# Kernel tuning notes

Measured on AMD Instinct MI355X. Metric: run time of the kernel, lower is better.

The kernel has to match this reference:

```python
import jax, jax.numpy as jnp
import numpy as np
import math

# Model hyperparameters (SchNet defaults)
H = 128        # hidden_channels
F = 128        # num_filters
G = 50         # num_gaussians
CUT = 6.0      # cutoff (Angstrom)
L_INT = 3      # num_interactions
# Graph scale
N_MOL = 512    # molecules
APM = 32       # atoms per molecule
N = N_MOL * APM
BOX = 10.0     # side of cubic box per molecule


def _ssp(x):
    # ShiftedSoftplus
    return jax.nn.softplus(x) - math.log(2.0)


def setup_inputs() -> dict:
    rng = np.random.default_rng(0)
    pos = rng.uniform(0.0, BOX, (N_MOL, APM, 3)).astype(np.float32)
    # radius graph within each molecule (faithful to radius_graph_custom,
    # precomputed here because edge count is data-dependent)
    srcs, dsts = [], []
    for m in range(N_MOL):
        p = pos[m]
        dm = np.linalg.norm(p[:, None, :] - p[None, :, :], axis=-1)
        mask = dm <= CUT
        np.fill_diagonal(mask, False)
        s, t = np.nonzero(mask)
        srcs.append(s + m * APM)
        dsts.append(t + m * APM)
    edge_index = np.stack([np.concatenate(srcs), np.concatenate(dsts)]).astype(np.int32)
    pos = pos.reshape(N, 3)
    batch = np.repeat(np.arange(N_MOL, dtype=np.int32), APM)
    z = rng.integers(1, 100, N).astype(np.int32)

    key = jax.random.key(0)
    ks = jax.random.split(key, 16)
    s = 0.1
    nrm = lambda k, shp: (jax.random.normal(k, shp, dtype=jnp.float32) * s)
    return {
        "z": jnp.asarray(z),
        "pos": jnp.asarray(pos),
        "batch": jnp.asarray(batch),
        "edge_index": jnp.asarray(edge_index),
        "emb": nrm(ks[0], (100, H)),
        "mlp_w1": nrm(ks[1], (L_INT, G, F)),
        "mlp_b1": jnp.zeros((L_INT, F), jnp.float32),
        "mlp_w2": nrm(ks[2], (L_INT, F, F)),
        "mlp_b2": jnp.zeros((L_INT, F), jnp.float32),
        "cf1_w": nrm(ks[3], (L_INT, H, F)),
        "cf2_w": nrm(ks[4], (L_INT, F, H)),
        "cf2_b": jnp.zeros((L_INT, H), jnp.float32),
        "lin_w": nrm(ks[5], (L_INT, H, H)),
        "lin_b": jnp.zeros((L_INT, H), jnp.float32),
        "out1_w": nrm(ks[6], (H, H // 2)),
        "out1_b": jnp.zeros((H // 2,), jnp.float32),
        "out2_w": nrm(ks[7], (H // 2, 1)),
        "out2_b": jnp.zeros((1,), jnp.float32),
    }


def reference(z, pos, batch, edge_index, emb,
              mlp_w1, mlp_b1, mlp_w2, mlp_b2,
              cf1_w, cf2_w, cf2_b, lin_w, lin_b,
              out1_w, out1_b, out2_w, out2_b):
    src, dst = edge_index[0], edge_index[1]
    # edge_weight = euclidean distance (== cdist[src, dst])
    d = jnp.sqrt(jnp.sum((pos[src] - pos[dst]) ** 2, axis=-1))  # [E]
    # GaussianSmearing
    offs = jnp.linspace(0.0, CUT, G)
    coeff = -0.5 / (CUT / (G - 1)) ** 2
    edge_attr = jnp.exp(coeff * (d[:, None] - offs[None, :]) ** 2)  # [E, G]
    # cosine cutoff
    Ccut = 0.5 * (jnp.cos(d * math.pi / CUT) + 1.0)  # [E]

    h = emb[z]  # [N, H]
    for l in range(L_INT):
        # edge filter MLP with cutoff
        W = _ssp(edge_attr @ mlp_w1[l] + mlp_b1[l]) @ mlp_w2[l] + mlp_b2[l]  # [E, F]
        W = W * Ccut[:, None]
        # CFConv: lin1 -> gather x_j -> multiply -> scatter-add to dst -> lin2
        msg = (h @ cf1_w[l])[src] * W                                # [E, F]
        agg = jax.ops.segment_sum(msg, dst, num_segments=N)          # [N, F]
        v = agg @ cf2_w[l] + cf2_b[l]                                # [N, H]
        v = _ssp(v)
        v = v @ lin_w[l] + lin_b[l]
        h = h + v  # residual

    h = _ssp(h @ out1_w + out1_b)
    h = h @ out2_w + out2_b                                          # [N, 1]
    out = jax.ops.segment_sum(h, batch, num_segments=N_MOL)          # [N_MOL, 1]
    return out
```

## Files before the change

kernel.cpp:

```cpp
#include <hip/hip_runtime.h>
#include <hip/hip_bf16.h>
#include <math.h>

#define NATOMS 16384
#define NMOL   512
#define APM    32
#define GDIM   50
#define KTAB   2048
#define MAXEPM 1000

#define STRH 132
#define STRA 136

typedef __attribute__((ext_vector_type(8))) short   short8;
typedef __attribute__((ext_vector_type(4))) float   floatx4;

__device__ __forceinline__ float ssp(float x) {
    float e = __expf(-fabsf(x));
    return fmaxf(x, 0.0f) + __logf(1.0f + e) - 0.69314718055994531f;
}

__device__ __forceinline__ unsigned short f2bf(float x) {
    union { float f; unsigned int u; } v; v.f = x;
    unsigned int lsb = (v.u >> 16) & 1u;
    v.u += 0x7fffu + lsb;
    return (unsigned short)(v.u >> 16);
}

__device__ __forceinline__ float bf2f(unsigned int u16bits) {
    union { unsigned int u; float f; } v; v.u = u16bits << 16;
    return v.f;
}

__device__ __forceinline__ unsigned int pk2bf(float a, float b) {
    __hip_bfloat162 h = __float22bfloat162_rn(make_float2(a, b));
    unsigned int u;
    __builtin_memcpy(&u, &h, 4);
    return u;
}

#define KW1 72
#define KW2 136
#define TILE_K 63
#define NTILE 33

__global__ __launch_bounds__(256) void mega_setup_kernel(
    const float* __restrict__ pos, const int* __restrict__ eidx, int E, int EB,
    int* __restrict__ rowptr,
    const float* __restrict__ cf1, const float* __restrict__ cf2,
    const float* __restrict__ lin, const float* __restrict__ out1,
    unsigned short* __restrict__ Wtall, uint2* __restrict__ meta,
    const float* __restrict__ w1_, const float* __restrict__ b1_,
    const float* __restrict__ w2_, const float* __restrict__ b2_,
    unsigned int* __restrict__ Tp)
{
    const int WB = (9 * 16384 + 64 * 128 + 255) / 256;
    const int b = blockIdx.x;
    const int tid = threadIdx.x;

    if (b < EB) {
        int idx = b * 256 + tid;
        if (idx < E) {
            int s = eidx[idx], t = eidx[E + idx];
            float dx = pos[3 * s]     - pos[3 * t];
            float dy = pos[3 * s + 1] - pos[3 * t + 1];
            float dz = pos[3 * s + 2] - pos[3 * t + 2];
            float d  = sqrtf(dx * dx + dy * dy + dz * dz);
            float u  = d * (float)(KTAB - 1) / 6.0f;
            int i = min((int)u, KTAB - 2);
            meta[idx] = make_uint2(((unsigned)i << 6) | (unsigned)(t & 31),
                                   __float_as_uint(u - (float)i));
        } else if (idx < E + NATOMS + 1) {
            int a = idx - E;
            if (a == 0) meta[E] = make_uint2(32u, 0u);
            int lo = 0, hi = E;
            while (lo < hi) { int mid = (lo + hi) >> 1; if (eidx[mid] < a) lo = mid + 1; else hi = mid; }
            rowptr[a] = lo;
        }
        return;
    }
    if (b < EB + WB) {
        int idx = (b - EB) * 256 + tid;
        if (idx < 9 * 16384) {
            int wi = idx >> 14, rem = idx & 16383;
            int n = rem >> 7, k = rem & 127;
            int l = wi / 3, which = wi % 3;
            const float* src = (which == 0) ? cf1 : (which == 1) ? cf2 : lin;
            Wtall[idx] = f2bf(src[(size_t)l * 16384 + k * 128 + n]);
        } else if (idx < 9 * 16384 + 64 * 128) {
            int q = idx - 9 * 16384;
            int n = q >> 7, k = q & 127;
            Wtall[idx] = f2bf(out1[k * 64 + n]);
        }
        return;
    }

    __shared__ unsigned short s_bufA[128 * KW2];
    __shared__ unsigned short s_bufB[128 * KW1];

    const int tt = b - EB - WB;
    const int l  = tt / NTILE;
    const int bx = tt % NTILE;
    const float* w1 = w1_ + (size_t)l * GDIM * 128;
    const float* b1 = b1_ + (size_t)l * 128;
    const float* w2 = w2_ + (size_t)l * 128 * 128;
    const float* b2 = b2_ + (size_t)l * 128;
    unsigned int* Tpg = Tp + (size_t)l * KTAB * 128;

    unsigned short* s_w1T = s_bufB;
    unsigned short* s_w2T = s_bufA;
    unsigned short* s_t   = s_bufB;

    for (int i = tid; i < GDIM * 128; i += 256) {
        int g = i >> 7, f = i & 127;
        s_w1T[f * KW1 + g] = f2bf(w1[i]);
    }
    for (int i = tid; i < (64 - GDIM) * 128; i += 256) {
        int g = GDIM + (i >> 7), f = i & 127;
        s_w1T[f * KW1 + g] = 0;
    }
    for (int i = tid; i < 128 * 128; i += 256) {
        int k = i >> 7, n = i & 127;
        s_w2T[n * KW2 + k] = f2bf(w2[i]);
    }

    const int lane = tid & 63;
    const int w    = tid >> 6;
    const int l15  = lane & 15;
    const int quad = lane >> 4;

    float b1v[8], b2v[8];
    #pragma unroll
    for (int nt = 0; nt < 8; nt++) {
        b1v[nt] = b1[nt * 16 + l15];
        b2v[nt] = b2[nt * 16 + l15];
    }
    __syncthreads();

    const float hstep = 6.0f / (float)(KTAB - 1);
    const float step  = 6.0f / 49.0f;
    const float coeff = -0.5f / (step * step);
    const float pioc  = 3.14159265358979323846f / 6.0f;
    const int k0 = bx * TILE_K;
    const float dm = (float)(k0 + w * 16 + l15) * hstep;

    floatx4 acc1[8];
    #pragma unroll
    for (int nt = 0; nt < 8; nt++) acc1[nt] = (floatx4){0.f, 0.f, 0.f, 0.f};
    #pragma unroll
    for (int ks = 0; ks < 2; ks++) {
        unsigned int ap[4];
        #pragma unroll
        for (int jj = 0; jj < 4; jj++) {
            int g0 = ks * 32 + quad * 8 + 2 * jj;
            float d0 = dm - (float)g0 * step;
            float d1 = dm - (float)(g0 + 1) * step;
            float v0 = (g0 < GDIM)     ? __expf(coeff * d0 * d0) : 0.0f;
            float v1 = (g0 + 1 < GDIM) ? __expf(coeff * d1 * d1) : 0.0f;
            ap[jj] = pk2bf(v0, v1);
        }
        short8 af;
        __builtin_memcpy(&af, ap, 16);
        #pragma unroll
        for (int nt = 0; nt < 8; nt++) {
            short8 bfg = *(const short8*)&s_w1T[(nt * 16 + l15) * KW1 + ks * 32 + quad * 8];
            acc1[nt] = __builtin_amdgcn_mfma_f32_16x16x32_bf16(af, bfg, acc1[nt], 0, 0, 0);
        }
    }
    __syncthreads();

    #pragma unroll
    for (int nt = 0; nt < 8; nt++) {
        #pragma unroll
        for (int r = 0; r < 4; r++) {
            int row = w * 16 + quad * 4 + r;
            s_t[row * KW2 + nt * 16 + l15] = f2bf(ssp(acc1[nt][r] + b1v[nt]));
        }
    }

    floatx4 acc2[8];
    #pragma unroll
    for (int nt = 0; nt < 8; nt++) acc2[nt] = (floatx4){0.f, 0.f, 0.f, 0.f};
    #pragma unroll
    for (int ks = 0; ks < 4; ks++) {
        short8 af = *(const short8*)&s_t[(w * 16 + l15) * KW2 + ks * 32 + quad * 8];
        #pragma unroll
        for (int nt = 0; nt < 8; nt++) {
            short8 bfg = *(const short8*)&s_w2T[(nt * 16 + l15) * KW2 + ks * 32 + quad * 8];
            acc2[nt] = __builtin_amdgcn_mfma_f32_16x16x32_bf16(af, bfg, acc2[nt], 0, 0, 0);
        }
    }

    unsigned short* T_lds = s_t;
    #pragma unroll
    for (int nt = 0; nt < 8; nt++) {
        #pragma unroll
        for (int r = 0; r < 4; r++) {
            int row = w * 16 + quad * 4 + r;
            float d = (float)(k0 + row) * hstep;
            float cut = 0.5f * (__cosf(d * pioc) + 1.0f);
            T_lds[row * KW2 + nt * 16 + l15] = f2bf((acc2[nt][r] + b2v[nt]) * cut);
        }
    }
    __syncthreads();

    for (int i = tid; i < TILE_K * 128; i += 256) {
        int r = i >> 7, f = i & 127;
        int k = k0 + r;
        if (k <= KTAB - 2) {
            unsigned int w0 = T_lds[r * KW2 + f];
            unsigned int w1b = T_lds[(r + 1) * KW2 + f];
            unsigned int dw = f2bf(bf2f(w1b) - bf2f(w0));
            Tpg[(size_t)k * 128 + f] = w0 | (dw << 16);
        }
    }
}

__global__ __launch_bounds__(512, 4) void fused_schnet_kernel(
    const int* __restrict__ z, const float* __restrict__ emb,
    const int* __restrict__ rowptr, const uint2* __restrict__ meta,
    const unsigned int* __restrict__ Tp,
    const unsigned short* __restrict__ Wtall,
    const float* __restrict__ cf2_b, const float* __restrict__ lin_b,
    const float* __restrict__ out1_b, const float* __restrict__ out2_w,
    const float* __restrict__ out2_b,
    float* __restrict__ out)
{
    __shared__ float s_h[32 * STRH];
    __shared__ float s_hx[33 * 128];
    __shared__ unsigned short s_agg[32 * STRA];
    __shared__ uint2 s_meta[MAXEPM];
    __shared__ float s_red;
    unsigned short* s_t = (unsigned short*)s_hx;

    const int tid  = threadIdx.x;
    const int lane = tid & 63;
    const int w    = tid >> 6;
    const int l15  = lane & 15;
    const int quad = lane >> 4;
    const int r16  = (w & 1) * 16;
    const int c32  = (w >> 1) * 32;
    const int pair = lane >> 5;
    const int c4   = (lane & 31) * 4;
    const int B0   = blockIdx.x * 32;

    for (int i = tid; i < 32 * 128; i += 512) {
        int row = i >> 7, col = i & 127;
        s_h[row * STRH + col] = emb[(size_t)z[B0 + row] * 128 + col];
    }
    if (tid < 128) s_hx[32 * 128 + tid] = 0.0f;
    if (tid == 0) s_red = 0.0f;

    const int ebase = rowptr[B0];
    const int nE    = rowptr[B0 + 32] - ebase;
    for (int i = tid; i < nE; i += 512) s_meta[i] = meta[ebase + i];
    if (tid == 0) s_meta[nE] = make_uint2(32u, 0u);

    const int rp = rowptr[B0 + w * 4 + min(lane, 4)] - ebase;

    const unsigned short* WtO = Wtall + 9 * 16384;

    for (int l = 0; l < 3; l++) {
        const unsigned short* W1 = Wtall + (size_t)(l * 3 + 0) * 16384;
        const unsigned short* W2 = Wtall + (size_t)(l * 3 + 1) * 16384;
        const unsigned short* W3 = Wtall + (size_t)(l * 3 + 2) * 16384;
        const unsigned int* Tpl  = Tp + (size_t)l * KTAB * 128;

        __syncthreads();

        floatx4 acc[2];
        #pragma unroll
        for (int nt = 0; nt < 2; nt++) acc[nt] = (floatx4){0.f, 0.f, 0.f, 0.f};
        #pragma unroll
        for (int ks = 0; ks < 4; ks++) {
            const float* hp = &s_h[(r16 + l15) * STRH + ks * 32 + quad * 8];
            float4 xa = *(const float4*)hp;
            float4 xb = *(const float4*)(hp + 4);
            unsigned int ap[4];
            ap[0] = pk2bf(xa.x, xa.y); ap[1] = pk2bf(xa.z, xa.w);
            ap[2] = pk2bf(xb.x, xb.y); ap[3] = pk2bf(xb.z, xb.w);
            short8 af;
            __builtin_memcpy(&af, ap, 16);
            #pragma unroll
            for (int nt = 0; nt < 2; nt++) {
                short8 bfg = *(const short8*)&W1[(size_t)(c32 + nt * 16 + l15) * 128 + ks * 32 + quad * 8];
                acc[nt] = __builtin_amdgcn_mfma_f32_16x16x32_bf16(af, bfg, acc[nt], 0, 0, 0);
            }
        }
        #pragma unroll
        for (int nt = 0; nt < 2; nt++) {
            #pragma unroll
            for (int r = 0; r < 4; r++)
                s_hx[(r16 + quad * 4 + r) * 128 + c32 + nt * 16 + l15] = acc[nt][r];
        }

        __syncthreads();

        for (int al = 0; al < 4; al++) {
            const int e0 = __shfl(rp, al);
            const int e1 = __shfl(rp, al + 1);
            float a0[8], a1[8], a2[8], a3[8];
            #pragma unroll
            for (int j = 0; j < 8; j++) { a0[j] = a1[j] = a2[j] = a3[j] = 0.f; }
            for (int e = e0; e < e1; e += 16) {
                #pragma unroll
                for (int j = 0; j < 8; j++) {
                    int idx = e + 2 * j + pair;
                    idx = (idx < e1) ? idx : nE;
                    uint2 q = s_meta[idx];
                    int tl   = q.x & 63;
                    int knot = q.x >> 6;
                    uint4 tp = *(const uint4*)&Tpl[(size_t)knot * 128 + c4];
                    float4 hv = *(const float4*)&s_hx[tl * 128 + c4];
                    float fr = __uint_as_float(q.y);
                    a0[j] = fmaf(hv.x, fmaf(fr, __uint_as_float(tp.x & 0xffff0000u),
                                            __uint_as_float(tp.x << 16)), a0[j]);
                    a1[j] = fmaf(hv.y, fmaf(fr, __uint_as_float(tp.y & 0xffff0000u),
                                            __uint_as_float(tp.y << 16)), a1[j]);
                    a2[j] = fmaf(hv.z, fmaf(fr, __uint_as_float(tp.z & 0xffff0000u),
                                            __uint_as_float(tp.z << 16)), a2[j]);
                    a3[j] = fmaf(hv.w, fmaf(fr, __uint_as_float(tp.w & 0xffff0000u),
                                            __uint_as_float(tp.w << 16)), a3[j]);
                }
            }
            float s0 = ((a0[0] + a0[1]) + (a0[2] + a0[3])) + ((a0[4] + a0[5]) + (a0[6] + a0[7]));
            float s1 = ((a1[0] + a1[1]) + (a1[2] + a1[3])) + ((a1[4] + a1[5]) + (a1[6] + a1[7]));
            float s2 = ((a2[0] + a2[1]) + (a2[2] + a2[3])) + ((a2[4] + a2[5]) + (a2[6] + a2[7]));
            float s3 = ((a3[0] + a3[1]) + (a3[2] + a3[3])) + ((a3[4] + a3[5]) + (a3[6] + a3[7]));
            s0 += __shfl_xor(s0, 32);
            s1 += __shfl_xor(s1, 32);
            s2 += __shfl_xor(s2, 32);
            s3 += __shfl_xor(s3, 32);
            if (pair == 0) {
                uint2 pkd = make_uint2(pk2bf(s0, s1), pk2bf(s2, s3));
                *(uint2*)&s_agg[(w * 4 + al) * STRA + c4] = pkd;
            }
        }

        __syncthreads();

        float bva[2], bvb[2];
        #pragma unroll
        for (int nt = 0; nt < 2; nt++) {
            bva[nt] = cf2_b[l * 128 + c32 + nt * 16 + l15];
            bvb[nt] = lin_b[l * 128 + c32 + nt * 16 + l15];
        }
        #pragma unroll
        for (int nt = 0; nt < 2; nt++) acc[nt] = (floatx4){0.f, 0.f, 0.f, 0.f};
        #pragma unroll
        for (int ks = 0; ks < 4; ks++) {
            short8 af = *(const short8*)&s_agg[(r16 + l15) * STRA + ks * 32 + quad * 8];
            #pragma unroll
            for (int nt = 0; nt < 2; nt++) {
                short8 bfg = *(const short8*)&W2[(size_t)(c32 + nt * 16 + l15) * 128 + ks * 32 + quad * 8];
                acc[nt] = __builtin_amdgcn_mfma_f32_16x16x32_bf16(af, bfg, acc[nt], 0, 0, 0);
            }
        }
        #pragma unroll
        for (int nt = 0; nt < 2; nt++) {
            #pragma unroll
            for (int r = 0; r < 4; r++) {
                int row = r16 + quad * 4 + r;
                s_t[row * STRA + c32 + nt * 16 + l15] = f2bf(ssp(acc[nt][r] + bva[nt]));
            }
        }

        __syncthreads();

        #pragma unroll
        for (int nt = 0; nt < 2; nt++) acc[nt] = (floatx4){0.f, 0.f, 0.f, 0.f};
        #pragma unroll
        for (int ks = 0; ks < 4; ks++) {
            short8 af = *(const short8*)&s_t[(r16 + l15) * STRA + ks * 32 + quad * 8];
            #pragma unroll
            for (int nt = 0; nt < 2; nt++) {
                short8 bfg = *(const short8*)&W3[(size_t)(c32 + nt * 16 + l15) * 128 + ks * 32 + quad * 8];
                acc[nt] = __builtin_amdgcn_mfma_f32_16x16x32_bf16(af, bfg, acc[nt], 0, 0, 0);
            }
        }
        #pragma unroll
        for (int nt = 0; nt < 2; nt++) {
            #pragma unroll
            for (int r = 0; r < 4; r++) {
                int row = r16 + quad * 4 + r;
                s_h[row * STRH + c32 + nt * 16 + l15] += acc[nt][r] + bvb[nt];
            }
        }
    }

    __syncthreads();

    const int c16 = (w >> 1) * 16;
    floatx4 ha = (floatx4){0.f, 0.f, 0.f, 0.f};
    #pragma unroll
    for (int ks = 0; ks < 4; ks++) {
        const float* hp = &s_h[(r16 + l15) * STRH + ks * 32 + quad * 8];
        float4 xa = *(const float4*)hp;
        float4 xb = *(const float4*)(hp + 4);
        unsigned int ap[4];
        ap[0] = pk2bf(xa.x, xa.y); ap[1] = pk2bf(xa.z, xa.w);
        ap[2] = pk2bf(xb.x, xb.y); ap[3] = pk2bf(xb.z, xb.w);
        short8 af;
        __builtin_memcpy(&af, ap, 16);
        short8 bfg = *(const short8*)&WtO[(size_t)(c16 + l15) * 128 + ks * 32 + quad * 8];
        ha = __builtin_amdgcn_mfma_f32_16x16x32_bf16(af, bfg, ha, 0, 0, 0);
    }
    float part = 0.0f;
    {
        float b1o = out1_b[c16 + l15];
        float o2  = out2_w[c16 + l15];
        #pragma unroll
        for (int r = 0; r < 4; r++)
            part += ssp(ha[r] + b1o) * o2;
    }
    #pragma unroll
    for (int off = 32; off > 0; off >>= 1) part += __shfl_down(part, off);
    if (lane == 0) atomicAdd(&s_red, part);
    __syncthreads();
    if (tid == 0) out[blockIdx.x] = s_red + 32.0f * out2_b[0];
}

extern "C" void kernel_launch(void* const* d_in, const int* in_sizes, int n_in,
                              void* d_out, int out_size, void* d_ws, size_t ws_size,
                              hipStream_t stream)
{
    const int*   z      = (const int*)d_in[0];
    const float* pos    = (const float*)d_in[1];
    const int*   eidx   = (const int*)d_in[3];
    const float* emb    = (const float*)d_in[4];
    const float* mlp_w1 = (const float*)d_in[5];
    const float* mlp_b1 = (const float*)d_in[6];
    const float* mlp_w2 = (const float*)d_in[7];
    const float* mlp_b2 = (const float*)d_in[8];
    const float* cf1_w  = (const float*)d_in[9];
    const float* cf2_w  = (const float*)d_in[10];
    const float* cf2_b  = (const float*)d_in[11];
    const float* lin_w  = (const float*)d_in[12];
    const float* lin_b  = (const float*)d_in[13];
    const float* out1_w = (const float*)d_in[14];
    const float* out1_b = (const float*)d_in[15];
    const float* out2_w = (const float*)d_in[16];
    const float* out2_b = (const float*)d_in[17];
    const int E = in_sizes[3] / 2;

    char* p = (char*)d_ws;
    uint2* meta = (uint2*)p;                      p += ((size_t)(E + 1) * 8 + 63) & ~63ULL;
    unsigned int* Tp = (unsigned int*)p;          p += (size_t)3 * KTAB * 128 * 4;
    int* rowptr = (int*)p;                        p += ((size_t)(NATOMS + 1) * 4 + 63) & ~63ULL;
    unsigned short* Wtall = (unsigned short*)p;

    const int EB = (E + NATOMS + 1 + 255) / 256;
    const int WB = (9 * 16384 + 64 * 128 + 255) / 256;
    const int TB = NTILE * 3;
    mega_setup_kernel<<<EB + WB + TB, 256, 0, stream>>>(
        pos, eidx, E, EB, rowptr, cf1_w, cf2_w, lin_w, out1_w, Wtall, meta,
        mlp_w1, mlp_b1, mlp_w2, mlp_b2, Tp);

    fused_schnet_kernel<<<NMOL, 512, 0, stream>>>(
        z, emb, rowptr, meta, Tp, Wtall,
        cf2_b, lin_b, out1_b, out2_w, out2_b, (float*)d_out);
}
```

Baseline: 180.7 us.

## Remap edge aggregation so each lane owns one atom across a 16-channel slice

The edge message aggregation is reorganised so that each lane handles one destination atom and each wave owns a 16-channel slice, instead of each wave processing four atoms with lanes spread over channels. Table loads for the next edge are software-prefetched one round ahead. The s_hx stride is padded to reduce LDS bank conflicts, and the per-atom edge ranges come from a warp-wide max so every lane runs the same number of rounds. The cost is divergence and idle lanes when atoms have uneven edge counts, higher register pressure from 16 accumulators plus prefetch buffers, and less coalesced table reads because each lane now reads a different knot row. The meta[E] sentinel write in the preprocess kernel is removed; the fused kernel still writes its own shared sentinel.

```diff
diff --git a/kernel.cpp b/kernel.cpp
--- a/kernel.cpp
+++ b/kernel.cpp
@@ -72,7 +72,6 @@
                                    __float_as_uint(u - (float)i));
         } else if (idx < E + NATOMS + 1) {
             int a = idx - E;
-            if (a == 0) meta[E] = make_uint2(32u, 0u);
             int lo = 0, hi = E;
             while (lo < hi) { int mid = (lo + hi) >> 1; if (eidx[mid] < a) lo = mid + 1; else hi = mid; }
             rowptr[a] = lo;
@@ -227,7 +226,7 @@
     float* __restrict__ out)
 {
     __shared__ float s_h[32 * STRH];
-    __shared__ float s_hx[33 * 128];
+    __shared__ float s_hx[33 * STRH];
     __shared__ unsigned short s_agg[32 * STRA];
     __shared__ uint2 s_meta[MAXEPM];
     __shared__ float s_red;
@@ -240,15 +239,16 @@
     const int quad = lane >> 4;
     const int r16  = (w & 1) * 16;
     const int c32  = (w >> 1) * 32;
+    const int cw   = w * 16;
+    const int atom = lane & 31;
     const int pair = lane >> 5;
-    const int c4   = (lane & 31) * 4;
     const int B0   = blockIdx.x * 32;
 
     for (int i = tid; i < 32 * 128; i += 512) {
         int row = i >> 7, col = i & 127;
         s_h[row * STRH + col] = emb[(size_t)z[B0 + row] * 128 + col];
     }
-    if (tid < 128) s_hx[32 * 128 + tid] = 0.0f;
+    if (tid < 128) s_hx[32 * STRH + tid] = 0.0f;
     if (tid == 0) s_red = 0.0f;
 
     const int ebase = rowptr[B0];
@@ -256,7 +256,13 @@
     for (int i = tid; i < nE; i += 512) s_meta[i] = meta[ebase + i];
     if (tid == 0) s_meta[nE] = make_uint2(32u, 0u);
 
-    const int rp = rowptr[B0 + w * 4 + min(lane, 4)] - ebase;
+    const int rp = rowptr[B0 + min(lane, 32)] - ebase;
+    const int e0 = __shfl(rp, atom);
+    const int e1 = __shfl(rp, atom + 1);
+    int md = e1 - e0;
+    #pragma unroll
+    for (int off = 1; off < 32; off <<= 1) md = max(md, __shfl_xor(md, off));
+    const int rounds = (md + 1) >> 1;
 
     const unsigned short* WtO = Wtall + 9 * 16384;
 
@@ -291,50 +297,61 @@
         for (int nt = 0; nt < 2; nt++) {
             #pragma unroll
             for (int r = 0; r < 4; r++)
-                s_hx[(r16 + quad * 4 + r) * 128 + c32 + nt * 16 + l15] = acc[nt][r];
+                s_hx[(r16 + quad * 4 + r) * STRH + c32 + nt * 16 + l15] = acc[nt][r];
         }
 
         __syncthreads();
 
-        for (int al = 0; al < 4; al++) {
-            const int e0 = __shfl(rp, al);
-            const int e1 = __shfl(rp, al + 1);
-            float a0[8], a1[8], a2[8], a3[8];
-            #pragma unroll
-            for (int j = 0; j < 8; j++) { a0[j] = a1[j] = a2[j] = a3[j] = 0.f; }
-            for (int e = e0; e < e1; e += 16) {
+        float ga[16];
+        #pragma unroll
+        for (int i = 0; i < 16; i++) ga[i] = 0.0f;
+        {
+            int e = e0 + pair;
+            int idx = (e < e1) ? e : nE;
+            uint2 q = s_meta[idx];
+            uint4 t0 = *(const uint4*)&Tpl[(size_t)(q.x >> 6) * 128 + cw];
+            uint4 t1 = *(const uint4*)&Tpl[(size_t)(q.x >> 6) * 128 + cw + 4];
+            uint4 t2 = *(const uint4*)&Tpl[(size_t)(q.x >> 6) * 128 + cw + 8];
+            uint4 t3 = *(const uint4*)&Tpl[(size_t)(q.x >> 6) * 128 + cw + 12];
+            for (int r = 0; r < rounds; r++) {
+                int en = e + 2;
+                int idxn = (en < e1) ? en : nE;
+                uint2 qn = s_meta[idxn];
+                uint4 n0 = *(const uint4*)&Tpl[(size_t)(qn.x >> 6) * 128 + cw];
+                uint4 n1 = *(const uint4*)&Tpl[(size_t)(qn.x >> 6) * 128 + cw + 4];
+                uint4 n2 = *(const uint4*)&Tpl[(size_t)(qn.x >> 6) * 128 + cw + 8];
+                uint4 n3 = *(const uint4*)&Tpl[(size_t)(qn.x >> 6) * 128 + cw + 12];
+                int tl = q.x & 63;
+                float fr = __uint_as_float(q.y);
+                const float* hp = &s_hx[tl * STRH + cw];
+                float4 h0 = *(const float4*)hp;
+                float4 h1 = *(const float4*)(hp + 4);
+                float4 h2 = *(const float4*)(hp + 8);
+                float4 h3 = *(const float4*)(hp + 12);
+                unsigned int tu[16];
+                *(uint4*)&tu[0] = t0; *(uint4*)&tu[4] = t1;
+                *(uint4*)&tu[8] = t2; *(uint4*)&tu[12] = t3;
+                float hv[16];
+                *(float4*)&hv[0] = h0; *(float4*)&hv[4] = h1;
+                *(float4*)&hv[8] = h2; *(float4*)&hv[12] = h3;
                 #pragma unroll
-                for (int j = 0; j < 8; j++) {
-                    int idx = e + 2 * j + pair;
-                    idx = (idx < e1) ? idx : nE;
-                    uint2 q = s_meta[idx];
-                    int tl   = q.x & 63;
-                    int knot = q.x >> 6;
-                    uint4 tp = *(const uint4*)&Tpl[(size_t)knot * 128 + c4];
-                    float4 hv = *(const float4*)&s_hx[tl * 128 + c4];
-                    float fr = __uint_as_float(q.y);
-                    a0[j] = fmaf(hv.x, fmaf(fr, __uint_as_float(tp.x & 0xffff0000u),
-                                            __uint_as_float(tp.x << 16)), a0[j]);
-                    a1[j] = fmaf(hv.y, fmaf(fr, __uint_as_float(tp.y & 0xffff0000u),
-                                            __uint_as_float(tp.y << 16)), a1[j]);
-                    a2[j] = fmaf(hv.z, fmaf(fr, __uint_as_float(tp.z & 0xffff0000u),
-                                            __uint_as_float(tp.z << 16)), a2[j]);
-                    a3[j] = fmaf(hv.w, fmaf(fr, __uint_as_float(tp.w & 0xffff0000u),
-                                            __uint_as_float(tp.w << 16)), a3[j]);
+                for (int i = 0; i < 16; i++) {
+                    float wv = fmaf(fr, __uint_as_float(tu[i] & 0xffff0000u),
+                                    __uint_as_float(tu[i] << 16));
+                    ga[i] = fmaf(hv[i], wv, ga[i]);
                 }
-            }
-            float s0 = ((a0[0] + a0[1]) + (a0[2] + a0[3])) + ((a0[4] + a0[5]) + (a0[6] + a0[7]));
-            float s1 = ((a1[0] + a1[1]) + (a1[2] + a1[3])) + ((a1[4] + a1[5]) + (a1[6] + a1[7]));
-            float s2 = ((a2[0] + a2[1]) + (a2[2] + a2[3])) + ((a2[4] + a2[5]) + (a2[6] + a2[7]));
-            float s3 = ((a3[0] + a3[1]) + (a3[2] + a3[3])) + ((a3[4] + a3[5]) + (a3[6] + a3[7]));
-            s0 += __shfl_xor(s0, 32);
-            s1 += __shfl_xor(s1, 32);
-            s2 += __shfl_xor(s2, 32);
-            s3 += __shfl_xor(s3, 32);
-            if (pair == 0) {
-                uint2 pkd = make_uint2(pk2bf(s0, s1), pk2bf(s2, s3));
-                *(uint2*)&s_agg[(w * 4 + al) * STRA + c4] = pkd;
-            }
+                q = qn; t0 = n0; t1 = n1; t2 = n2; t3 = n3; e = en;
+            }
+        }
+        #pragma unroll
+        for (int i = 0; i < 16; i++) ga[i] += __shfl_xor(ga[i], 32);
+        if (pair == 0) {
+            unsigned int pk[8];
+            #pragma unroll
+            for (int i = 0; i < 8; i++) pk[i] = pk2bf(ga[2 * i], ga[2 * i + 1]);
+            uint4* dst = (uint4*)&s_agg[atom * STRA + cw];
+            dst[0] = *(uint4*)&pk[0];
+            dst[1] = *(uint4*)&pk[4];
         }
 
         __syncthreads();
```

Result: slower. 199.8 us (+10.6%).

## Replace linear-interpolated filter table with denser nearest-knot lookup

Applied to the files above, without the earlier changes.

Doubles the distance-table resolution to 4096 knots and drops linear interpolation, storing plain bf16 filter values and a 4-byte per-edge metadata word holding the rounded knot index. The gather loop in the fused kernel now has each lane handle two channels of one edge at a time, with no fraction multiply and no cross-half-wave shuffle reduction. This halves the table and metadata bytes per edge and shortens the inner loop. In exchange it adds a nearest-neighbour approximation error in the filter, doubles the setup tiles to build, and uses narrower 4-byte loads per lane.

```diff
diff --git a/kernel.cpp b/kernel.cpp
--- a/kernel.cpp
+++ b/kernel.cpp
@@ -6,7 +6,7 @@
 #define NMOL   512
 #define APM    32
 #define GDIM   50
-#define KTAB   2048
+#define KTAB   4096
 #define MAXEPM 1000
 
 #define STRH 132
@@ -27,11 +27,6 @@
     return (unsigned short)(v.u >> 16);
 }
 
-__device__ __forceinline__ float bf2f(unsigned int u16bits) {
-    union { unsigned int u; float f; } v; v.u = u16bits << 16;
-    return v.f;
-}
-
 __device__ __forceinline__ unsigned int pk2bf(float a, float b) {
     __hip_bfloat162 h = __float22bfloat162_rn(make_float2(a, b));
     unsigned int u;
@@ -41,18 +36,17 @@
 
 #define KW1 72
 #define KW2 136
-#define TILE_K 63
-#define NTILE 33
+#define NTILE (KTAB / 64)
 
 __global__ __launch_bounds__(256) void mega_setup_kernel(
     const float* __restrict__ pos, const int* __restrict__ eidx, int E, int EB,
     int* __restrict__ rowptr,
     const float* __restrict__ cf1, const float* __restrict__ cf2,
     const float* __restrict__ lin, const float* __restrict__ out1,
-    unsigned short* __restrict__ Wtall, uint2* __restrict__ meta,
+    unsigned short* __restrict__ Wtall, unsigned int* __restrict__ meta,
     const float* __restrict__ w1_, const float* __restrict__ b1_,
     const float* __restrict__ w2_, const float* __restrict__ b2_,
-    unsigned int* __restrict__ Tp)
+    unsigned short* __restrict__ Tt)
 {
     const int WB = (9 * 16384 + 64 * 128 + 255) / 256;
     const int b = blockIdx.x;
@@ -67,12 +61,10 @@
             float dz = pos[3 * s + 2] - pos[3 * t + 2];
             float d  = sqrtf(dx * dx + dy * dy + dz * dz);
             float u  = d * (float)(KTAB - 1) / 6.0f;
-            int i = min((int)u, KTAB - 2);
-            meta[idx] = make_uint2(((unsigned)i << 6) | (unsigned)(t & 31),
-                                   __float_as_uint(u - (float)i));
+            int i = min((int)(u + 0.5f), KTAB - 1);
+            meta[idx] = ((unsigned)i << 6) | (unsigned)(t & 31);
         } else if (idx < E + NATOMS + 1) {
             int a = idx - E;
-            if (a == 0) meta[E] = make_uint2(32u, 0u);
             int lo = 0, hi = E;
             while (lo < hi) { int mid = (lo + hi) >> 1; if (eidx[mid] < a) lo = mid + 1; else hi = mid; }
             rowptr[a] = lo;
@@ -105,7 +97,7 @@
     const float* b1 = b1_ + (size_t)l * 128;
     const float* w2 = w2_ + (size_t)l * 128 * 128;
     const float* b2 = b2_ + (size_t)l * 128;
-    unsigned int* Tpg = Tp + (size_t)l * KTAB * 128;
+    unsigned short* Tg = Tt + (size_t)l * KTAB * 128;
 
     unsigned short* s_w1T = s_bufB;
     unsigned short* s_w2T = s_bufA;
@@ -141,7 +133,7 @@
     const float step  = 6.0f / 49.0f;
     const float coeff = -0.5f / (step * step);
     const float pioc  = 3.14159265358979323846f / 6.0f;
-    const int k0 = bx * TILE_K;
+    const int k0 = bx * 64;
     const float dm = (float)(k0 + w * 16 + l15) * hstep;
 
     floatx4 acc1[8];
@@ -191,7 +183,6 @@
         }
     }
 
-    unsigned short* T_lds = s_t;
     #pragma unroll
     for (int nt = 0; nt < 8; nt++) {
         #pragma unroll
@@ -199,27 +190,15 @@
             int row = w * 16 + quad * 4 + r;
             float d = (float)(k0 + row) * hstep;
             float cut = 0.5f * (__cosf(d * pioc) + 1.0f);
-            T_lds[row * KW2 + nt * 16 + l15] = f2bf((acc2[nt][r] + b2v[nt]) * cut);
-        }
-    }
-    __syncthreads();
-
-    for (int i = tid; i < TILE_K * 128; i += 256) {
-        int r = i >> 7, f = i & 127;
-        int k = k0 + r;
-        if (k <= KTAB - 2) {
-            unsigned int w0 = T_lds[r * KW2 + f];
-            unsigned int w1b = T_lds[(r + 1) * KW2 + f];
-            unsigned int dw = f2bf(bf2f(w1b) - bf2f(w0));
-            Tpg[(size_t)k * 128 + f] = w0 | (dw << 16);
+            Tg[(size_t)(k0 + row) * 128 + nt * 16 + l15] = f2bf((acc2[nt][r] + b2v[nt]) * cut);
         }
     }
 }
 
 __global__ __launch_bounds__(512, 4) void fused_schnet_kernel(
     const int* __restrict__ z, const float* __restrict__ emb,
-    const int* __restrict__ rowptr, const uint2* __restrict__ meta,
-    const unsigned int* __restrict__ Tp,
+    const int* __restrict__ rowptr, const unsigned int* __restrict__ meta,
+    const unsigned short* __restrict__ Tt,
     const unsigned short* __restrict__ Wtall,
     const float* __restrict__ cf2_b, const float* __restrict__ lin_b,
     const float* __restrict__ out1_b, const float* __restrict__ out2_w,
@@ -229,7 +208,7 @@
     __shared__ float s_h[32 * STRH];
     __shared__ float s_hx[33 * 128];
     __shared__ unsigned short s_agg[32 * STRA];
-    __shared__ uint2 s_meta[MAXEPM];
+    __shared__ unsigned int s_meta[MAXEPM];
     __shared__ float s_red;
     unsigned short* s_t = (unsigned short*)s_hx;
 
@@ -240,8 +219,6 @@
     const int quad = lane >> 4;
     const int r16  = (w & 1) * 16;
     const int c32  = (w >> 1) * 32;
-    const int pair = lane >> 5;
-    const int c4   = (lane & 31) * 4;
     const int B0   = blockIdx.x * 32;
 
     for (int i = tid; i < 32 * 128; i += 512) {
@@ -254,7 +231,7 @@
     const int ebase = rowptr[B0];
     const int nE    = rowptr[B0 + 32] - ebase;
     for (int i = tid; i < nE; i += 512) s_meta[i] = meta[ebase + i];
-    if (tid == 0) s_meta[nE] = make_uint2(32u, 0u);
+    if (tid == 0) s_meta[nE] = 32u;
 
     const int rp = rowptr[B0 + w * 4 + min(lane, 4)] - ebase;
 
@@ -264,7 +241,7 @@
         const unsigned short* W1 = Wtall + (size_t)(l * 3 + 0) * 16384;
         const unsigned short* W2 = Wtall + (size_t)(l * 3 + 1) * 16384;
         const unsigned short* W3 = Wtall + (size_t)(l * 3 + 2) * 16384;
-        const unsigned int* Tpl  = Tp + (size_t)l * KTAB * 128;
+        const unsigned short* Ttl = Tt + (size_t)l * KTAB * 128;
 
         __syncthreads();
 
@@ -299,42 +276,25 @@
         for (int al = 0; al < 4; al++) {
             const int e0 = __shfl(rp, al);
             const int e1 = __shfl(rp, al + 1);
-            float a0[8], a1[8], a2[8], a3[8];
-            #pragma unroll
-            for (int j = 0; j < 8; j++) { a0[j] = a1[j] = a2[j] = a3[j] = 0.f; }
-            for (int e = e0; e < e1; e += 16) {
+            float ax[8], ay[8];
+            #pragma unroll
+            for (int j = 0; j < 8; j++) { ax[j] = 0.f; ay[j] = 0.f; }
+            for (int e = e0; e < e1; e += 8) {
                 #pragma unroll
                 for (int j = 0; j < 8; j++) {
-                    int idx = e + 2 * j + pair;
-                    idx = (idx < e1) ? idx : nE;
-                    uint2 q = s_meta[idx];
-                    int tl   = q.x & 63;
-                    int knot = q.x >> 6;
-                    uint4 tp = *(const uint4*)&Tpl[(size_t)knot * 128 + c4];
-                    float4 hv = *(const float4*)&s_hx[tl * 128 + c4];
-                    float fr = __uint_as_float(q.y);
-                    a0[j] = fmaf(hv.x, fmaf(fr, __uint_as_float(tp.x & 0xffff0000u),
-                                            __uint_as_float(tp.x << 16)), a0[j]);
-                    a1[j] = fmaf(hv.y, fmaf(fr, __uint_as_float(tp.y & 0xffff0000u),
-                                            __uint_as_float(tp.y << 16)), a1[j]);
-                    a2[j] = fmaf(hv.z, fmaf(fr, __uint_as_float(tp.z & 0xffff0000u),
-                                            __uint_as_float(tp.z << 16)), a2[j]);
-                    a3[j] = fmaf(hv.w, fmaf(fr, __uint_as_float(tp.w & 0xffff0000u),
-                                            __uint_as_float(tp.w << 16)), a3[j]);
+                    int idx = (e + j < e1) ? (e + j) : nE;
+                    unsigned int q = s_meta[idx];
+                    int tl   = q & 63;
+                    int knot = q >> 6;
+                    unsigned int tp = *(const unsigned int*)&Ttl[((size_t)knot << 7) + 2 * lane];
+                    float2 hv = *(const float2*)&s_hx[(tl << 7) + 2 * lane];
+                    ax[j] = fmaf(hv.x, __uint_as_float(tp << 16), ax[j]);
+                    ay[j] = fmaf(hv.y, __uint_as_float(tp & 0xffff0000u), ay[j]);
                 }
             }
-            float s0 = ((a0[0] + a0[1]) + (a0[2] + a0[3])) + ((a0[4] + a0[5]) + (a0[6] + a0[7]));
-            float s1 = ((a1[0] + a1[1]) + (a1[2] + a1[3])) + ((a1[4] + a1[5]) + (a1[6] + a1[7]));
-            float s2 = ((a2[0] + a2[1]) + (a2[2] + a2[3])) + ((a2[4] + a2[5]) + (a2[6] + a2[7]));
-            float s3 = ((a3[0] + a3[1]) + (a3[2] + a3[3])) + ((a3[4] + a3[5]) + (a3[6] + a3[7]));
-            s0 += __shfl_xor(s0, 32);
-            s1 += __shfl_xor(s1, 32);
-            s2 += __shfl_xor(s2, 32);
-            s3 += __shfl_xor(s3, 32);
-            if (pair == 0) {
-                uint2 pkd = make_uint2(pk2bf(s0, s1), pk2bf(s2, s3));
-                *(uint2*)&s_agg[(w * 4 + al) * STRA + c4] = pkd;
-            }
+            float sx = ((ax[0] + ax[1]) + (ax[2] + ax[3])) + ((ax[4] + ax[5]) + (ax[6] + ax[7]));
+            float sy = ((ay[0] + ay[1]) + (ay[2] + ay[3])) + ((ay[4] + ay[5]) + (ay[6] + ay[7]));
+            *(unsigned int*)&s_agg[(w * 4 + al) * STRA + 2 * lane] = pk2bf(sx, sy);
         }
 
         __syncthreads();
@@ -444,8 +404,8 @@
     const int E = in_sizes[3] / 2;
 
     char* p = (char*)d_ws;
-    uint2* meta = (uint2*)p;                      p += ((size_t)(E + 1) * 8 + 63) & ~63ULL;
-    unsigned int* Tp = (unsigned int*)p;          p += (size_t)3 * KTAB * 128 * 4;
+    unsigned int* meta = (unsigned int*)p;        p += ((size_t)(E + 1) * 4 + 63) & ~63ULL;
+    unsigned short* Tt = (unsigned short*)p;      p += (size_t)3 * KTAB * 128 * 2;
     int* rowptr = (int*)p;                        p += ((size_t)(NATOMS + 1) * 4 + 63) & ~63ULL;
     unsigned short* Wtall = (unsigned short*)p;
 
@@ -454,9 +414,9 @@
     const int TB = NTILE * 3;
     mega_setup_kernel<<<EB + WB + TB, 256, 0, stream>>>(
         pos, eidx, E, EB, rowptr, cf1_w, cf2_w, lin_w, out1_w, Wtall, meta,
-        mlp_w1, mlp_b1, mlp_w2, mlp_b2, Tp);
+        mlp_w1, mlp_b1, mlp_w2, mlp_b2, Tt);
 
     fused_schnet_kernel<<<NMOL, 512, 0, stream>>>(
-        z, emb, rowptr, meta, Tp, Wtall,
+        z, emb, rowptr, meta, Tt, Wtall,
         cf2_b, lin_b, out1_b, out2_w, out2_b, (float*)d_out);
 }
```

Result: faster. 169.1 us (median of 2 runs) (-6.4%).
